# Kernel tuning notes

Hardware: AMD Instinct MI355X
Metric: run time of the kernel (lower is better)

The kernel has to match this reference:

```python
import jax, jax.numpy as jnp
import numpy as np

NUM_BITS = 16
BIT_START = 96
VALUE_DIM = 96  # E.DIM in the original code: the value payload slice [0:96)


def setup_inputs() -> dict:
    key = jax.random.key(0)
    B, S, D = 8, 32768, 128
    x = jax.random.normal(key, (B, S, D), dtype=jnp.float32)
    return {"x": x, "query_addr": 12345}


def reference(x, query_addr):
    # query_addr is a static Python int -> decompose into NUM_BITS binary bits
    query_bits = jnp.array([(query_addr >> k) & 1 for k in range(NUM_BITS)],
                           dtype=x.dtype)  # [NUM_BITS]
    key_bits = x[:, :, BIT_START:BIT_START + NUM_BITS]          # [B, S, NUM_BITS]
    match = 1.0 - jnp.abs(key_bits - query_bits)                # broadcast over [B, S]
    attention_weights = jnp.prod(match, axis=-1)                # [B, S]
    values = x[:, :, :VALUE_DIM]                                # [B, S, VALUE_DIM]
    output = jnp.einsum('bs,bsd->bd', attention_weights, values)  # [B, VALUE_DIM]
    return output
```

## Files before the change

kernel.cpp:

```cpp
#include <hip/hip_runtime.h>


constexpr int B = 8;
constexpr int S = 32768;
constexpr int D4 = 32;
constexpr int VAL4 = 24;
constexpr int ROWS_PER_STEP = 8;
constexpr int BLOCKS_PER_B = 256;
constexpr int SPB = S / BLOCKS_PER_B;

__global__ __launch_bounds__(256)
void bma_stage1(const float* __restrict__ x, const int* __restrict__ qaddr,
                float* __restrict__ partial) {
    const int t    = threadIdx.x;
    const int c    = t & 31;
    const int rg   = t >> 5;
    const int lane = t & 63;
    const int b    = blockIdx.x / BLOCKS_PER_B;
    const int s0   = (blockIdx.x % BLOCKS_PER_B) * SPB;

    const unsigned qa = (unsigned)qaddr[0];
    float qb0 = 0.f, qb1 = 0.f, qb2 = 0.f, qb3 = 0.f;
    if (c >= 24 && c < 28) {
        const int k0 = (c - 24) * 4;
        qb0 = (float)((qa >> (k0 + 0)) & 1u);
        qb1 = (float)((qa >> (k0 + 1)) & 1u);
        qb2 = (float)((qa >> (k0 + 2)) & 1u);
        qb3 = (float)((qa >> (k0 + 3)) & 1u);
    }

    const float4* __restrict__ xb =
        reinterpret_cast<const float4*>(x) + (long)b * S * D4;
    const int src = (lane & 32) | 24;

    float4 acc = make_float4(0.f, 0.f, 0.f, 0.f);

    #pragma unroll 4
    for (int i = 0; i < SPB / ROWS_PER_STEP; ++i) {
        const int s = s0 + rg + i * ROWS_PER_STEP;
        float4 v = make_float4(0.f, 0.f, 0.f, 0.f);
        if (c < 28) v = xb[(long)s * D4 + c];

        float p = 1.0f;
        if (c >= 24 && c < 28) {
            p = (1.0f - fabsf(v.x - qb0)) * (1.0f - fabsf(v.y - qb1)) *
                (1.0f - fabsf(v.z - qb2)) * (1.0f - fabsf(v.w - qb3));
        }
        p *= __shfl_xor(p, 1);
        p *= __shfl_xor(p, 2);
        const float w = __shfl(p, src, 64);

        if (c < VAL4) {
            acc.x = fmaf(w, v.x, acc.x);
            acc.y = fmaf(w, v.y, acc.y);
            acc.z = fmaf(w, v.z, acc.z);
            acc.w = fmaf(w, v.w, acc.w);
        }
    }

    __shared__ float4 red[256];
    red[t] = acc;
    __syncthreads();
    if (t < 32) {
        float4 sum = red[t];
        #pragma unroll
        for (int g = 1; g < 8; ++g) {
            float4 o = red[t + 32 * g];
            sum.x += o.x; sum.y += o.y; sum.z += o.z; sum.w += o.w;
        }
        if (t < VAL4) {
            float4* pp = reinterpret_cast<float4*>(partial) + (long)blockIdx.x * VAL4 + t;
            *pp = sum;
        }
    }
}

__global__ __launch_bounds__(256)
void bma_stage2(const float* __restrict__ partial, float* __restrict__ out) {
    const int t  = threadIdx.x;
    const int c  = t & 31;
    const int rg = t >> 5;
    const int b  = blockIdx.x;

    const float4* __restrict__ pp =
        reinterpret_cast<const float4*>(partial) + (long)b * BLOCKS_PER_B * VAL4;

    float4 acc = make_float4(0.f, 0.f, 0.f, 0.f);
    if (c < VAL4) {
        #pragma unroll 4
        for (int chunk = rg; chunk < BLOCKS_PER_B; chunk += ROWS_PER_STEP) {
            float4 v = pp[(long)chunk * VAL4 + c];
            acc.x += v.x; acc.y += v.y; acc.z += v.z; acc.w += v.w;
        }
    }

    __shared__ float4 red[256];
    red[t] = acc;
    __syncthreads();
    if (t < VAL4) {
        float4 sum = red[t];
        #pragma unroll
        for (int g = 1; g < 8; ++g) {
            float4 o = red[t + 32 * g];
            sum.x += o.x; sum.y += o.y; sum.z += o.z; sum.w += o.w;
        }
        reinterpret_cast<float4*>(out)[(long)b * VAL4 + t] = sum;
    }
}

extern "C" void kernel_launch(void* const* d_in, const int* in_sizes, int n_in,
                              void* d_out, int out_size, void* d_ws, size_t ws_size,
                              hipStream_t stream) {
    const float* x   = (const float*)d_in[0];
    const int*   qa  = (const int*)d_in[1];
    float*       out = (float*)d_out;
    float*       ws  = (float*)d_ws;

    bma_stage1<<<dim3(B * BLOCKS_PER_B), dim3(256), 0, stream>>>(x, qa, ws);
    bma_stage2<<<dim3(B), dim3(256), 0, stream>>>(ws, out);
}
```

Measured before the change: 193.5 us.

## Split stage1 into weight-compute pass in LDS and fully-busy value accumulation pass

Stage1 is restructured into two phases. First, pairs of threads compute each row's 16-bit match product and store the weights in shared memory. Then every thread accumulates three float4 value columns over rows using those weights, so no lanes sit idle and the per-row shuffles are gone. The cost is a second read of the key columns, an extra barrier and a larger 32-way LDS reduction; the kernel is memory-bound, so the benefit depends on better load efficiency.

```diff
diff --git a/kernel.cpp b/kernel.cpp
--- a/kernel.cpp
+++ b/kernel.cpp
@@ -5,73 +5,80 @@
 constexpr int S = 32768;
 constexpr int D4 = 32;
 constexpr int VAL4 = 24;
-constexpr int ROWS_PER_STEP = 8;
 constexpr int BLOCKS_PER_B = 256;
 constexpr int SPB = S / BLOCKS_PER_B;
+constexpr int ROWS_PER_ITER = 32;
+constexpr int P2_ITERS = SPB / ROWS_PER_ITER;
 
 __global__ __launch_bounds__(256)
 void bma_stage1(const float* __restrict__ x, const int* __restrict__ qaddr,
                 float* __restrict__ partial) {
-    const int t    = threadIdx.x;
-    const int c    = t & 31;
-    const int rg   = t >> 5;
-    const int lane = t & 63;
-    const int b    = blockIdx.x / BLOCKS_PER_B;
-    const int s0   = (blockIdx.x % BLOCKS_PER_B) * SPB;
-
-    const unsigned qa = (unsigned)qaddr[0];
-    float qb0 = 0.f, qb1 = 0.f, qb2 = 0.f, qb3 = 0.f;
-    if (c >= 24 && c < 28) {
-        const int k0 = (c - 24) * 4;
-        qb0 = (float)((qa >> (k0 + 0)) & 1u);
-        qb1 = (float)((qa >> (k0 + 1)) & 1u);
-        qb2 = (float)((qa >> (k0 + 2)) & 1u);
-        qb3 = (float)((qa >> (k0 + 3)) & 1u);
-    }
+    const int t  = threadIdx.x;
+    const int b  = blockIdx.x / BLOCKS_PER_B;
+    const int s0 = (blockIdx.x % BLOCKS_PER_B) * SPB;
 
     const float4* __restrict__ xb =
         reinterpret_cast<const float4*>(x) + (long)b * S * D4;
-    const int src = (lane & 32) | 24;
 
-    float4 acc = make_float4(0.f, 0.f, 0.f, 0.f);
+    __shared__ float  wlds[SPB];
+    __shared__ float4 red[32][VAL4 + 1];
 
-    #pragma unroll 4
-    for (int i = 0; i < SPB / ROWS_PER_STEP; ++i) {
-        const int s = s0 + rg + i * ROWS_PER_STEP;
-        float4 v = make_float4(0.f, 0.f, 0.f, 0.f);
-        if (c < 28) v = xb[(long)s * D4 + c];
+    {
+        const unsigned qa  = (unsigned)qaddr[0];
+        const int row  = t >> 1;
+        const int h    = t & 1;
+        const long rb  = (long)(s0 + row) * D4;
+        const float4 k0 = xb[rb + 24 + 2 * h];
+        const float4 k1 = xb[rb + 25 + 2 * h];
+        const int base = h * 8;
+        float p = 1.0f;
+        p *= 1.0f - fabsf(k0.x - (float)((qa >> (base + 0)) & 1u));
+        p *= 1.0f - fabsf(k0.y - (float)((qa >> (base + 1)) & 1u));
+        p *= 1.0f - fabsf(k0.z - (float)((qa >> (base + 2)) & 1u));
+        p *= 1.0f - fabsf(k0.w - (float)((qa >> (base + 3)) & 1u));
+        p *= 1.0f - fabsf(k1.x - (float)((qa >> (base + 4)) & 1u));
+        p *= 1.0f - fabsf(k1.y - (float)((qa >> (base + 5)) & 1u));
+        p *= 1.0f - fabsf(k1.z - (float)((qa >> (base + 6)) & 1u));
+        p *= 1.0f - fabsf(k1.w - (float)((qa >> (base + 7)) & 1u));
+        p *= __shfl_xor(p, 1);
+        if (h == 0) wlds[row] = p;
+    }
+    __syncthreads();
 
-        float p = 1.0f;
-        if (c >= 24 && c < 28) {
-            p = (1.0f - fabsf(v.x - qb0)) * (1.0f - fabsf(v.y - qb1)) *
-                (1.0f - fabsf(v.z - qb2)) * (1.0f - fabsf(v.w - qb3));
-        }
-        p *= __shfl_xor(p, 1);
-        p *= __shfl_xor(p, 2);
-        const float w = __shfl(p, src, 64);
+    const int f  = t & 7;
+    const int rg = t >> 3;
+    float4 a0 = make_float4(0.f, 0.f, 0.f, 0.f);
+    float4 a1 = a0, a2 = a0;
 
-        if (c < VAL4) {
-            acc.x = fmaf(w, v.x, acc.x);
-            acc.y = fmaf(w, v.y, acc.y);
-            acc.z = fmaf(w, v.z, acc.z);
-            acc.w = fmaf(w, v.w, acc.w);
-        }
+    #pragma unroll
+    for (int i = 0; i < P2_ITERS; ++i) {
+        const int  row  = i * ROWS_PER_ITER + rg;
+        const long base = (long)(s0 + row) * D4;
+        const float4 v0 = xb[base + f];
+        const float4 v1 = xb[base + f + 8];
+        const float4 v2 = xb[base + f + 16];
+        const float  w  = wlds[row];
+        a0.x = fmaf(w, v0.x, a0.x); a0.y = fmaf(w, v0.y, a0.y);
+        a0.z = fmaf(w, v0.z, a0.z); a0.w = fmaf(w, v0.w, a0.w);
+        a1.x = fmaf(w, v1.x, a1.x); a1.y = fmaf(w, v1.y, a1.y);
+        a1.z = fmaf(w, v1.z, a1.z); a1.w = fmaf(w, v1.w, a1.w);
+        a2.x = fmaf(w, v2.x, a2.x); a2.y = fmaf(w, v2.y, a2.y);
+        a2.z = fmaf(w, v2.z, a2.z); a2.w = fmaf(w, v2.w, a2.w);
     }
 
-    __shared__ float4 red[256];
-    red[t] = acc;
+    red[rg][f]      = a0;
+    red[rg][f + 8]  = a1;
+    red[rg][f + 16] = a2;
     __syncthreads();
-    if (t < 32) {
-        float4 sum = red[t];
-        #pragma unroll
-        for (int g = 1; g < 8; ++g) {
-            float4 o = red[t + 32 * g];
+
+    if (t < VAL4) {
+        float4 sum = make_float4(0.f, 0.f, 0.f, 0.f);
+        #pragma unroll 8
+        for (int g = 0; g < 32; ++g) {
+            const float4 o = red[g][t];
             sum.x += o.x; sum.y += o.y; sum.z += o.z; sum.w += o.w;
         }
-        if (t < VAL4) {
-            float4* pp = reinterpret_cast<float4*>(partial) + (long)blockIdx.x * VAL4 + t;
-            *pp = sum;
-        }
+        reinterpret_cast<float4*>(partial)[(long)blockIdx.x * VAL4 + t] = sum;
     }
 }
 
@@ -88,8 +95,8 @@
     float4 acc = make_float4(0.f, 0.f, 0.f, 0.f);
     if (c < VAL4) {
         #pragma unroll 4
-        for (int chunk = rg; chunk < BLOCKS_PER_B; chunk += ROWS_PER_STEP) {
-            float4 v = pp[(long)chunk * VAL4 + c];
+        for (int chunk = rg; chunk < BLOCKS_PER_B; chunk += 8) {
+            const float4 v = pp[(long)chunk * VAL4 + c];
             acc.x += v.x; acc.y += v.y; acc.z += v.z; acc.w += v.w;
         }
     }
@@ -101,7 +108,7 @@
         float4 sum = red[t];
         #pragma unroll
         for (int g = 1; g < 8; ++g) {
-            float4 o = red[t + 32 * g];
+            const float4 o = red[t + 32 * g];
             sum.x += o.x; sum.y += o.y; sum.z += o.z; sum.w += o.w;
         }
         reinterpret_cast<float4*>(out)[(long)b * VAL4 + t] = sum;
```

Measured after the change: 193.9 us (median of 2 runs). No clear change (+0.2%).
